# Optimization experiments

Measured on AMD Instinct MI355X. Metric: run time of the kernel, lower is better.

## Reference

```python
import jax, jax.numpy as jnp
import numpy as np

NUM_USERS = 1_000_000
NUM_ITEMS = 500_000
LATENT_DIM = 64
NUM_SAMPLE = 10
N_PAIRS = 131_072
PADDING_NUM = -2.0 ** 32 + 1


def setup_inputs() -> dict:
    key = jax.random.key(0)
    ks = jax.random.split(key, 11)
    return {
        "users": jax.random.randint(ks[0], (N_PAIRS,), 0, NUM_USERS),
        "items": jax.random.randint(ks[1], (N_PAIRS,), 0, NUM_ITEMS),
        "sampled_user": jax.random.randint(ks[2], (NUM_USERS, NUM_SAMPLE), 0, NUM_USERS),
        "embedding_user": 0.1 * jax.random.normal(ks[3], (NUM_USERS, LATENT_DIM), dtype=jnp.float32),
        "embedding_item": 0.1 * jax.random.normal(ks[4], (NUM_ITEMS, LATENT_DIM), dtype=jnp.float32),
        "W_w": jax.random.normal(ks[5], (LATENT_DIM, LATENT_DIM), dtype=jnp.float32) * (1.0 / np.sqrt(LATENT_DIM)),
        "W_b": jax.random.normal(ks[6], (LATENT_DIM,), dtype=jnp.float32) * 0.01,
        "U_w": jax.random.normal(ks[7], (LATENT_DIM, LATENT_DIM), dtype=jnp.float32) * (1.0 / np.sqrt(LATENT_DIM)),
        "U_b": jax.random.normal(ks[8], (LATENT_DIM,), dtype=jnp.float32) * 0.01,
        "b": jax.random.normal(ks[9], (1, LATENT_DIM), dtype=jnp.float32),
        "v": jax.random.normal(ks[10], (LATENT_DIM,), dtype=jnp.float32),
    }


def reference(users, items, sampled_user, embedding_user, embedding_item,
              W_w, W_b, U_w, U_b, b, v):
    # CMN.helper(users, items)
    S = sampled_user.shape[1]
    adj_idx = sampled_user[users]                     # [N, S] irregular gather
    adj = embedding_user[adj_idx]                     # [N, S, D]
    M = embedding_user[users]                         # [N, D]
    I = embedding_item[items]                         # [N, D]
    # torch: sum over dim=1 of bmm(repeat(M),adjT)+bmm(repeat(I),adjT)
    #      == S * (M + I) . adj_j   (rows of repeated tensor are identical)
    q = S * jnp.einsum('nd,nsd->ns', M + I, adj)      # [N, S]
    q = jnp.where(q != 0, q, jnp.float32(PADDING_NUM))
    w = jax.nn.softmax(q, axis=1)                     # attention over S=10 neighbors
    o = jnp.einsum('ns,nsd->nd', w, adj)              # [N, D]
    pre = (M * I) @ U_w.T + U_b + o @ W_w.T + W_b + b  # [N, D]
    R = v * jax.nn.leaky_relu(pre, negative_slope=0.2)
    return jnp.sum(R, axis=1)                         # [N]
```

## Files before the change

### kernel.cpp

```cpp
#include <hip/hip_runtime.h>

#define NSAMP 10
#define PAD_NUM (-4294967295.0f)

typedef __attribute__((ext_vector_type(8))) short short8;
typedef __attribute__((ext_vector_type(4))) float f32x4;
typedef __attribute__((ext_vector_type(4))) int i32x4;

template<int CTRL>
__device__ __forceinline__ float dpp_add(float x) {
    int t = __builtin_amdgcn_update_dpp(0, __float_as_int(x), CTRL, 0xF, 0xF, true);
    return x + __int_as_float(t);
}

__device__ __forceinline__ float row_reduce16(float x) {
    x = dpp_add<0xB1>(x);
    x = dpp_add<0x4E>(x);
    x = dpp_add<0x141>(x);
    x = dpp_add<0x140>(x);
    return x;
}

__device__ __forceinline__ unsigned cvt_pk_bf16(float a, float b) {
    unsigned r;
    asm("v_cvt_pk_bf16_f32 %0, %1, %2" : "=v"(r) : "v"(a), "v"(b));
    return r;
}

__global__ __launch_bounds__(256, 5) void cmn_kernel(
    const int* __restrict__ users, const int* __restrict__ items,
    const int* __restrict__ sampled, const float* __restrict__ emb_u,
    const float* __restrict__ emb_i, const float* __restrict__ W_w,
    const float* __restrict__ W_b, const float* __restrict__ U_w,
    const float* __restrict__ U_b, const float* __restrict__ bvec,
    const float* __restrict__ vvec, float* __restrict__ out)
{
    __shared__ __align__(16) char sB[64 * 256];
    __shared__ __align__(16) char sA4[4][16 * 256];

    const int tid  = threadIdx.x;
    const int lane = tid & 63;
    const int wid  = tid >> 6;
    const int j    = lane & 15;
    const int g    = lane >> 4;
    char* myA = sA4[wid];

    #pragma unroll
    for (int i2 = 0; i2 < 4; ++i2) {
        const int e  = i2 * 256 + tid;
        const int d  = e >> 4;
        const int t0 = (e & 15) * 4;
        const f32x4 u4 = *reinterpret_cast<const f32x4*>(U_w + d * 64 + t0);
        const f32x4 w4 = *reinterpret_cast<const f32x4*>(W_w + d * 64 + t0);
        i32x4 pk;
        pk.x = cvt_pk_bf16(u4.x, w4.x);
        pk.y = cvt_pk_bf16(u4.y, w4.y);
        pk.z = cvt_pk_bf16(u4.z, w4.z);
        pk.w = cvt_pk_bf16(u4.w, w4.w);
        const int byteoff = (d * 256 + 4 * t0) ^ ((d & 7) << 4);
        *reinterpret_cast<i32x4*>(sB + byteoff) = pk;
    }

    const int base_pair = (blockIdx.x * 4 + wid) * 16;

    int u_cur  = users[base_pair + g];
    int it_cur = items[base_pair + g];
    int sidx[NSAMP];
    #pragma unroll
    for (int s = 0; s < NSAMP; ++s) sidx[s] = sampled[u_cur * NSAMP + s];

    #pragma unroll 1
    for (int c = 0; c < 4; ++c) {
        const f32x4 M4 = *reinterpret_cast<const f32x4*>(emb_u + (size_t)u_cur * 64 + 4 * j);
        const f32x4 I4 = *reinterpret_cast<const f32x4*>(emb_i + (size_t)it_cur * 64 + 4 * j);
        f32x4 adj[NSAMP];
        #pragma unroll
        for (int s = 0; s < NSAMP; ++s)
            adj[s] = *reinterpret_cast<const f32x4*>(emb_u + (size_t)sidx[s] * 64 + 4 * j);

        int u_nxt = 0, it_nxt = 0;
        int sidx_n[NSAMP] = {0, 0, 0, 0, 0, 0, 0, 0, 0, 0};
        if (c < 3) {
            u_nxt  = users[base_pair + (c + 1) * 4 + g];
            it_nxt = items[base_pair + (c + 1) * 4 + g];
            #pragma unroll
            for (int s = 0; s < NSAMP; ++s) sidx_n[s] = sampled[u_nxt * NSAMP + s];
        }

        const f32x4 sv4 = M4 + I4;
        const f32x4 mi4 = M4 * I4;

        float q[NSAMP];
        #pragma unroll
        for (int s = 0; s < NSAMP; ++s) {
            float d4 = sv4.x * adj[s].x;
            d4 = fmaf(sv4.y, adj[s].y, d4);
            d4 = fmaf(sv4.z, adj[s].z, d4);
            d4 = fmaf(sv4.w, adj[s].w, d4);
            q[s] = row_reduce16(d4);
        }
        float m = PAD_NUM;
        #pragma unroll
        for (int s = 0; s < NSAMP; ++s) {
            float qv = 10.0f * q[s];
            qv = (qv != 0.0f) ? qv : PAD_NUM;
            q[s] = qv;
            m = fmaxf(m, qv);
        }
        float esum = 0.0f;
        f32x4 o4 = {0.f, 0.f, 0.f, 0.f};
        #pragma unroll
        for (int s = 0; s < NSAMP; ++s) {
            const float e = __expf(q[s] - m);
            esum += e;
            o4.x = fmaf(e, adj[s].x, o4.x);
            o4.y = fmaf(e, adj[s].y, o4.y);
            o4.z = fmaf(e, adj[s].z, o4.z);
            o4.w = fmaf(e, adj[s].w, o4.w);
        }
        const float rcp = 1.0f / esum;

        i32x4 pk;
        pk.x = cvt_pk_bf16(mi4.x, o4.x * rcp);
        pk.y = cvt_pk_bf16(mi4.y, o4.y * rcp);
        pk.z = cvt_pk_bf16(mi4.z, o4.z * rcp);
        pk.w = cvt_pk_bf16(mi4.w, o4.w * rcp);
        const int prow = c * 4 + g;
        const int off  = (prow * 256 + 16 * j) ^ ((prow & 7) << 4);
        *reinterpret_cast<i32x4*>(myA + off) = pk;

        u_cur = u_nxt;
        it_cur = it_nxt;
        #pragma unroll
        for (int s = 0; s < NSAMP; ++s) sidx[s] = sidx_n[s];
    }

    __syncthreads();

    float biasArr[4], vArr[4];
    const int arow = lane & 15;
    const int kg   = lane >> 4;
    #pragma unroll
    for (int t = 0; t < 4; ++t) {
        const int dcol = t * 16 + arow;
        biasArr[t] = U_b[dcol] + W_b[dcol] + bvec[dcol];
        vArr[t]    = vvec[dcol];
    }

    short8 afr[4];
    #pragma unroll
    for (int ks = 0; ks < 4; ++ks) {
        const int off = (arow * 256 + ks * 64 + kg * 16) ^ ((arow & 7) << 4);
        afr[ks] = *reinterpret_cast<const short8*>(myA + off);
    }

    float ps0 = 0.f, ps1 = 0.f, ps2 = 0.f, ps3 = 0.f;
    #pragma unroll
    for (int t = 0; t < 4; ++t) {
        f32x4 acc = {0.f, 0.f, 0.f, 0.f};
        #pragma unroll
        for (int ks = 0; ks < 4; ++ks) {
            const int brow = t * 16 + arow;
            const int off = (brow * 256 + ks * 64 + kg * 16) ^ ((brow & 7) << 4);
            const short8 bfr = *reinterpret_cast<const short8*>(sB + off);
            acc = __builtin_amdgcn_mfma_f32_16x16x32_bf16(afr[ks], bfr, acc, 0, 0, 0);
        }
        #pragma unroll
        for (int r = 0; r < 4; ++r) {
            const float pre = acc[r] + biasArr[t];
            float val = vArr[t] * (pre >= 0.f ? pre : 0.2f * pre);
            val = row_reduce16(val);
            if      (r == 0) ps0 += val;
            else if (r == 1) ps1 += val;
            else if (r == 2) ps2 += val;
            else             ps3 += val;
        }
    }

    const int c4 = lane & 15;
    const float val = (c4 == 0) ? ps0 : (c4 == 1) ? ps1 : (c4 == 2) ? ps2 : ps3;
    if (c4 < 4) out[base_pair + kg * 4 + c4] = val;
}

extern "C" void kernel_launch(void* const* d_in, const int* in_sizes, int n_in,
                              void* d_out, int out_size, void* d_ws, size_t ws_size,
                              hipStream_t stream) {
    const int*   users   = (const int*)d_in[0];
    const int*   items   = (const int*)d_in[1];
    const int*   sampled = (const int*)d_in[2];
    const float* emb_u   = (const float*)d_in[3];
    const float* emb_i   = (const float*)d_in[4];
    const float* W_w     = (const float*)d_in[5];
    const float* W_b     = (const float*)d_in[6];
    const float* U_w     = (const float*)d_in[7];
    const float* U_b     = (const float*)d_in[8];
    const float* bvec    = (const float*)d_in[9];
    const float* vvec    = (const float*)d_in[10];
    float* out = (float*)d_out;

    const int blocks = 131072 / 64;
    cmn_kernel<<<dim3(blocks), dim3(256), 0, stream>>>(
        users, items, sampled, emb_u, emb_i, W_w, W_b, U_w, U_b, bvec, vvec, out);
}
```

Measured before the change: 67.16 us.

## Double-buffer embedding gathers across chunks with manual unrolled software pipeline

Replaces the rolled four-chunk loop with a fully unrolled two-stage pipeline. The embedding rows for the next chunk are gathered into a second register buffer while the current chunk's attention is computed, and sched_barrier calls pin that ordering. This keeps more gathers in flight per wave to hide memory latency. It doubles the register footprint, so launch bounds drop from 5 to 3 waves-per-EU occupancy hint, trading occupancy for memory-level parallelism per wave.

```diff
diff --git a/kernel.cpp b/kernel.cpp
--- a/kernel.cpp
+++ b/kernel.cpp
@@ -27,7 +27,60 @@
     return r;
 }
 
-__global__ __launch_bounds__(256, 5) void cmn_kernel(
+__device__ __forceinline__ void compute_chunk(
+    const f32x4 M4, const f32x4 I4, const f32x4* adj,
+    char* myA, const int prow, const int j)
+{
+    const f32x4 sv4 = M4 + I4;
+    const f32x4 mi4 = M4 * I4;
+
+    float q[NSAMP];
+    #pragma unroll
+    for (int s = 0; s < NSAMP; ++s) {
+        float d4 = sv4.x * adj[s].x;
+        d4 = fmaf(sv4.y, adj[s].y, d4);
+        d4 = fmaf(sv4.z, adj[s].z, d4);
+        d4 = fmaf(sv4.w, adj[s].w, d4);
+        q[s] = row_reduce16(d4);
+    }
+    float m = PAD_NUM;
+    #pragma unroll
+    for (int s = 0; s < NSAMP; ++s) {
+        float qv = 10.0f * q[s];
+        qv = (qv != 0.0f) ? qv : PAD_NUM;
+        q[s] = qv;
+        m = fmaxf(m, qv);
+    }
+    float esum = 0.0f;
+    f32x4 o4 = {0.f, 0.f, 0.f, 0.f};
+    #pragma unroll
+    for (int s = 0; s < NSAMP; ++s) {
+        const float e = __expf(q[s] - m);
+        esum += e;
+        o4.x = fmaf(e, adj[s].x, o4.x);
+        o4.y = fmaf(e, adj[s].y, o4.y);
+        o4.z = fmaf(e, adj[s].z, o4.z);
+        o4.w = fmaf(e, adj[s].w, o4.w);
+    }
+    const float rcp = 1.0f / esum;
+
+    i32x4 pk;
+    pk.x = cvt_pk_bf16(mi4.x, o4.x * rcp);
+    pk.y = cvt_pk_bf16(mi4.y, o4.y * rcp);
+    pk.z = cvt_pk_bf16(mi4.z, o4.z * rcp);
+    pk.w = cvt_pk_bf16(mi4.w, o4.w * rcp);
+    const int off = (prow * 256 + 16 * j) ^ ((prow & 7) << 4);
+    *reinterpret_cast<i32x4*>(myA + off) = pk;
+}
+
+#define LOAD_DATA(Mv, Iv, adjv, uu, ii, sx)                                         \
+    Mv = *reinterpret_cast<const f32x4*>(emb_u + (size_t)(uu) * 64 + 4 * j);        \
+    Iv = *reinterpret_cast<const f32x4*>(emb_i + (size_t)(ii) * 64 + 4 * j);        \
+    _Pragma("unroll")                                                                \
+    for (int s = 0; s < NSAMP; ++s)                                                  \
+        adjv[s] = *reinterpret_cast<const f32x4*>(emb_u + (size_t)(sx)[s] * 64 + 4 * j);
+
+__global__ __launch_bounds__(256, 3) void cmn_kernel(
     const int* __restrict__ users, const int* __restrict__ items,
     const int* __restrict__ sampled, const float* __restrict__ emb_u,
     const float* __restrict__ emb_i, const float* __restrict__ W_w,
@@ -63,77 +116,37 @@
 
     const int base_pair = (blockIdx.x * 4 + wid) * 16;
 
-    int u_cur  = users[base_pair + g];
-    int it_cur = items[base_pair + g];
-    int sidx[NSAMP];
-    #pragma unroll
-    for (int s = 0; s < NSAMP; ++s) sidx[s] = sampled[u_cur * NSAMP + s];
-
-    #pragma unroll 1
-    for (int c = 0; c < 4; ++c) {
-        const f32x4 M4 = *reinterpret_cast<const f32x4*>(emb_u + (size_t)u_cur * 64 + 4 * j);
-        const f32x4 I4 = *reinterpret_cast<const f32x4*>(emb_i + (size_t)it_cur * 64 + 4 * j);
-        f32x4 adj[NSAMP];
-        #pragma unroll
-        for (int s = 0; s < NSAMP; ++s)
-            adj[s] = *reinterpret_cast<const f32x4*>(emb_u + (size_t)sidx[s] * 64 + 4 * j);
-
-        int u_nxt = 0, it_nxt = 0;
-        int sidx_n[NSAMP] = {0, 0, 0, 0, 0, 0, 0, 0, 0, 0};
-        if (c < 3) {
-            u_nxt  = users[base_pair + (c + 1) * 4 + g];
-            it_nxt = items[base_pair + (c + 1) * 4 + g];
-            #pragma unroll
-            for (int s = 0; s < NSAMP; ++s) sidx_n[s] = sampled[u_nxt * NSAMP + s];
-        }
-
-        const f32x4 sv4 = M4 + I4;
-        const f32x4 mi4 = M4 * I4;
-
-        float q[NSAMP];
-        #pragma unroll
-        for (int s = 0; s < NSAMP; ++s) {
-            float d4 = sv4.x * adj[s].x;
-            d4 = fmaf(sv4.y, adj[s].y, d4);
-            d4 = fmaf(sv4.z, adj[s].z, d4);
-            d4 = fmaf(sv4.w, adj[s].w, d4);
-            q[s] = row_reduce16(d4);
-        }
-        float m = PAD_NUM;
-        #pragma unroll
-        for (int s = 0; s < NSAMP; ++s) {
-            float qv = 10.0f * q[s];
-            qv = (qv != 0.0f) ? qv : PAD_NUM;
-            q[s] = qv;
-            m = fmaxf(m, qv);
-        }
-        float esum = 0.0f;
-        f32x4 o4 = {0.f, 0.f, 0.f, 0.f};
-        #pragma unroll
-        for (int s = 0; s < NSAMP; ++s) {
-            const float e = __expf(q[s] - m);
-            esum += e;
-            o4.x = fmaf(e, adj[s].x, o4.x);
-            o4.y = fmaf(e, adj[s].y, o4.y);
-            o4.z = fmaf(e, adj[s].z, o4.z);
-            o4.w = fmaf(e, adj[s].w, o4.w);
-        }
-        const float rcp = 1.0f / esum;
-
-        i32x4 pk;
-        pk.x = cvt_pk_bf16(mi4.x, o4.x * rcp);
-        pk.y = cvt_pk_bf16(mi4.y, o4.y * rcp);
-        pk.z = cvt_pk_bf16(mi4.z, o4.z * rcp);
-        pk.w = cvt_pk_bf16(mi4.w, o4.w * rcp);
-        const int prow = c * 4 + g;
-        const int off  = (prow * 256 + 16 * j) ^ ((prow & 7) << 4);
-        *reinterpret_cast<i32x4*>(myA + off) = pk;
-
-        u_cur = u_nxt;
-        it_cur = it_nxt;
-        #pragma unroll
-        for (int s = 0; s < NSAMP; ++s) sidx[s] = sidx_n[s];
-    }
+    const int u0 = users[base_pair + g],      u1 = users[base_pair + 4 + g];
+    const int u2 = users[base_pair + 8 + g],  u3 = users[base_pair + 12 + g];
+    const int i0 = items[base_pair + g],      i1 = items[base_pair + 4 + g];
+    const int i2 = items[base_pair + 8 + g],  i3 = items[base_pair + 12 + g];
+
+    int sx0[NSAMP], sx1[NSAMP];
+    #pragma unroll
+    for (int s = 0; s < NSAMP; ++s) sx0[s] = sampled[u0 * NSAMP + s];
+    #pragma unroll
+    for (int s = 0; s < NSAMP; ++s) sx1[s] = sampled[u1 * NSAMP + s];
+
+    f32x4 MA, IA, adjA[NSAMP], MB, IB, adjB[NSAMP];
+    LOAD_DATA(MA, IA, adjA, u0, i0, sx0)
+    LOAD_DATA(MB, IB, adjB, u1, i1, sx1)
+    #pragma unroll
+    for (int s = 0; s < NSAMP; ++s) sx0[s] = sampled[u2 * NSAMP + s];
+    __builtin_amdgcn_sched_barrier(0);
+
+    compute_chunk(MA, IA, adjA, myA, 0 * 4 + g, j);
+    LOAD_DATA(MA, IA, adjA, u2, i2, sx0)
+    #pragma unroll
+    for (int s = 0; s < NSAMP; ++s) sx1[s] = sampled[u3 * NSAMP + s];
+    __builtin_amdgcn_sched_barrier(0);
+
+    compute_chunk(MB, IB, adjB, myA, 1 * 4 + g, j);
+    LOAD_DATA(MB, IB, adjB, u3, i3, sx1)
+    __builtin_amdgcn_sched_barrier(0);
+
+    compute_chunk(MA, IA, adjA, myA, 2 * 4 + g, j);
+    __builtin_amdgcn_sched_barrier(0);
+    compute_chunk(MB, IB, adjB, myA, 3 * 4 + g, j);
 
     __syncthreads();
 
```

After: 65.54 us. 1.02x faster.
